# Kernel tuning notes

Hardware: AMD Instinct MI355X
Metric: run time of the kernel (lower is better)

Reference implementation:

```python
import jax, jax.numpy as jnp
import numpy as np

NUM_BLOCKS = 16  # 4x4 grid of 2x2 blocks over the 8x8 matrix
E_BLK, H_BLK = 4, 2
E_CROSS, H_CROSS = 64, 8
VOCAB = 32000
LN_EPS = 1e-5


def _mha(x, Wqkv, bqkv, Wo, bo, nheads):
    """torch nn.MultiheadAttention (batch_first, self-attn, eval mode).
    Returns (out [B,T,E], attn weights averaged over heads [B,T,T])."""
    B, T, E = x.shape
    Dh = E // nheads
    qkv = x @ Wqkv.T + bqkv                      # [B,T,3E]
    q, k, v = jnp.split(qkv, 3, axis=-1)
    sp = lambda t: t.reshape(B, T, nheads, Dh).transpose(0, 2, 1, 3)  # [B,H,T,Dh]
    q, k, v = sp(q), sp(k), sp(v)
    scale = 1.0 / float(np.sqrt(Dh))
    scores = jnp.einsum('bhqd,bhkd->bhqk', q, k) * scale
    attn = jax.nn.softmax(scores, axis=-1)
    out = jnp.einsum('bhqk,bhkd->bhqd', attn, v).transpose(0, 2, 1, 3).reshape(B, T, E)
    return out @ Wo.T + bo, attn.mean(axis=1)


def _layernorm(x, g, b):
    mu = x.mean(-1, keepdims=True)
    var = x.var(-1, keepdims=True)
    return (x - mu) * jax.lax.rsqrt(var + LN_EPS) * g + b


def _to_blocks(M):
    # [B,T,8,8] -> [B,T,16,4]; block i = (row_blk*4+col_blk), 2x2 flattened row-major
    B, T = M.shape[:2]
    return jnp.transpose(M.reshape(B, T, 4, 2, 4, 2), (0, 1, 2, 4, 3, 5)).reshape(B, T, 16, 4)


def _from_blocks(x):
    # [B,T,16,4] -> [B,T,8,8]
    B, T = x.shape[:2]
    return jnp.transpose(x.reshape(B, T, 4, 4, 2, 2), (0, 1, 2, 4, 3, 5)).reshape(B, T, 8, 8)


def setup_inputs() -> dict:
    key = jax.random.key(0)
    ks = jax.random.split(key, 24)
    B, T = 4, 1024
    s = 0.05
    return {
        'M': jax.random.normal(ks[0], (B, T, 8, 8), jnp.float32),
        'token_ids': jax.random.randint(ks[1], (B, T), 0, VOCAB, jnp.int64),
        # 16 per-block MHA param sets (stacked)
        'Wqkv_blk': jax.random.normal(ks[2], (NUM_BLOCKS, 3 * E_BLK, E_BLK), jnp.float32) * s,
        'bqkv_blk': jnp.zeros((NUM_BLOCKS, 3 * E_BLK), jnp.float32),
        'Wo_blk': jax.random.normal(ks[3], (NUM_BLOCKS, E_BLK, E_BLK), jnp.float32) * s,
        'bo_blk': jnp.zeros((NUM_BLOCKS, E_BLK), jnp.float32),
        # cross-block MHA
        'Wqkv_c': jax.random.normal(ks[4], (3 * E_CROSS, E_CROSS), jnp.float32) * s,
        'bqkv_c': jnp.zeros((3 * E_CROSS,), jnp.float32),
        'Wo_c': jax.random.normal(ks[5], (E_CROSS, E_CROSS), jnp.float32) * s,
        'bo_c': jnp.zeros((E_CROSS,), jnp.float32),
        # FFN 64 -> 256 -> 64
        'W1': jax.random.normal(ks[6], (256, 64), jnp.float32) * s,
        'b1': jnp.zeros((256,), jnp.float32),
        'W2': jax.random.normal(ks[7], (64, 256), jnp.float32) * s,
        'b2': jnp.zeros((64,), jnp.float32),
        # LayerNorms
        'g1': jnp.ones((64,), jnp.float32), 'be1': jnp.zeros((64,), jnp.float32),
        'g2': jnp.ones((64,), jnp.float32), 'be2': jnp.zeros((64,), jnp.float32),
        # DynamicBlockSensitivity params
        'sens_emb': jax.random.normal(ks[8], (VOCAB, NUM_BLOCKS), jnp.float32) * s,
        'sens_alpha': jax.random.normal(ks[9], (NUM_BLOCKS,), jnp.float32) * s,
    }


def reference(M, token_ids, Wqkv_blk, bqkv_blk, Wo_blk, bo_blk,
              Wqkv_c, bqkv_c, Wo_c, bo_c, W1, b1, W2, b2,
              g1, be1, g2, be2, sens_emb, sens_alpha):
    B, T = M.shape[:2]
    blocks = _to_blocks(M)                                # [B,T,16,4]
    x_blk = jnp.moveaxis(blocks, 2, 0)                    # [16,B,T,4]
    blk_out, _ = jax.vmap(lambda x, W, b, Wo, bo: _mha(x, W, b, Wo, bo, H_BLK))(
        x_blk, Wqkv_blk, bqkv_blk, Wo_blk, bo_blk)        # [16,B,T,4]
    all_blocks = jnp.moveaxis(blk_out, 0, 2).reshape(B, T, 64)
    cross_out, attn_w = _mha(all_blocks, Wqkv_c, bqkv_c, Wo_c, bo_c, H_CROSS)
    all_blocks = _layernorm(all_blocks + cross_out, g1, be1)
    ffn = jax.nn.gelu(all_blocks @ W1.T + b1, approximate=False) @ W2.T + b2
    all_blocks = _layernorm(all_blocks + ffn, g2, be2)
    # Dynamic block sensitivity: token embedding + attention-received modulation
    attn_recv = attn_w.mean(axis=1)                       # [B,T] attention each token receives
    sens = jax.nn.sigmoid(sens_emb[token_ids] + attn_recv[..., None] * sens_alpha)  # [B,T,16]
    new_blocks = blocks + (all_blocks.reshape(B, T, 16, 4) - blocks) * sens[..., None]
    return _from_blocks(new_blocks)
```

## Files before the change

kernel.cpp:

```cpp
#include <hip/hip_runtime.h>
#include <hip/hip_bf16.h>
#include <math.h>

#define BB 4
#define TT 1024
#define BT 4096

#define OFF_BLOCKS 0
#define OFF_QKVB   262144
#define OFF_RECVP  262144
#define OFF_ALLB   1048576
#define OFF_QKVC   1310720
#define OFF_LC     2097152
#define OFF_ACCC   2129920
#define OFF_LN1    2396160
#define OFF_PARAMS 2658304
#define WS_FLOATS  2708624

#define P_W1T    0
#define P_W2T    16384
#define P_WQCT   32768
#define P_WOCT   45056
#define P_WOBLK  49152
#define P_BOBLK  49408
#define P_BQC    49472
#define P_BOC    49664
#define P_G1     49728
#define P_BE1    49792
#define P_B1     49856
#define P_B2     50112
#define P_G2     50176
#define P_BE2    50240
#define P_SAL    50304
#define P_TOTAL  50320

__device__ inline float rcpf(float x) { return __builtin_amdgcn_rcpf(x); }

typedef _Float16 h2 __attribute__((ext_vector_type(2)));
typedef __fp16   fh2 __attribute__((ext_vector_type(2)));
typedef _Float16 h8v __attribute__((ext_vector_type(8)));
typedef float    f4v __attribute__((ext_vector_type(4)));

__device__ inline uint pkh(float a, float b) {
#if __has_builtin(__builtin_amdgcn_cvt_pkrtz)
  fh2 r = __builtin_amdgcn_cvt_pkrtz(a, b);
  return __builtin_bit_cast(uint, r);
#else
  h2 r = { (_Float16)a, (_Float16)b };
  return __builtin_bit_cast(uint, r);
#endif
}
__device__ inline h2 toh2(uint u) { return __builtin_bit_cast(h2, u); }

__device__ inline bool detect_bf16(const void* M) {
  const unsigned short* h = (const unsigned short*)M;
  unsigned short v = h[threadIdx.x & 63];
  int e = (v >> 7) & 0xff;
  unsigned long long m = __ballot((e >= 90) && (e <= 141));
  return __popcll(m) >= 58;
}

template <bool ISBF>
__device__ inline float ldf(const void* p, int i) {
  if (ISBF) return __bfloat162float(((const __hip_bfloat16*)p)[i]);
  else      return ((const float*)p)[i];
}

template <bool ISBF>
__device__ void prep2_body(
    const void* M, const void* Wqkv_blk, const void* bqkv_blk,
    const void* W1, const void* W2, const void* Wqkv_c, const void* Wo_c,
    const void* Wo_blk, const void* bo_blk, const void* bqkv_c, const void* bo_c,
    const void* g1, const void* be1, const void* b1, const void* b2,
    const void* g2, const void* be2, const void* sens_al,
    float* blocks, float* qkv_blk, float* params) {
  if (blockIdx.x < 256) {
    int g = blockIdx.x * 256 + threadIdx.x;
    int i = g >> 12, bt = g & 4095;
    int rb = i >> 2, cb = i & 3;
    float x[4];
    #pragma unroll
    for (int r = 0; r < 2; ++r)
      #pragma unroll
      for (int c = 0; c < 2; ++c)
        x[r*2+c] = ldf<ISBF>(M, bt*64 + (rb*2+r)*8 + cb*2 + c);
    float* bo = blocks + bt*64 + i*4;
    #pragma unroll
    for (int j = 0; j < 4; ++j) bo[j] = x[j];
    float* o = qkv_blk + (i*BT + bt) * 12;
    #pragma unroll
    for (int c = 0; c < 12; ++c) {
      float a = ldf<ISBF>(bqkv_blk, i*12 + c);
      #pragma unroll
      for (int j = 0; j < 4; ++j) a += ldf<ISBF>(Wqkv_blk, i*48 + c*4 + j) * x[j];
      o[c] = a;
    }
  } else {
    for (int o = (blockIdx.x - 256)*256 + threadIdx.x; o < P_TOTAL; o += 16*256) {
      float v;
      if      (o < 16384) { int j = o >> 8, h2_ = o & 255; v = ldf<ISBF>(W1, h2_*64 + j); }
      else if (o < 32768) { int q = o - 16384; int k = q >> 6, j = q & 63; v = ldf<ISBF>(W2, j*256 + k); }
      else if (o < 45056) { int q = o - 32768; int j = q / 192, c = q % 192; v = ldf<ISBF>(Wqkv_c, c*64 + j); }
      else if (o < 49152) { int q = o - 45056; int m = q >> 6, j = q & 63; v = ldf<ISBF>(Wo_c, j*64 + m); }
      else if (o < 49408) v = ldf<ISBF>(Wo_blk, o - 49152);
      else if (o < 49472) v = ldf<ISBF>(bo_blk, o - 49408);
      else if (o < 49664) v = ldf<ISBF>(bqkv_c, o - 49472);
      else if (o < 49728) v = ldf<ISBF>(bo_c,   o - 49664);
      else if (o < 49792) v = ldf<ISBF>(g1,     o - 49728);
      else if (o < 49856) v = ldf<ISBF>(be1,    o - 49792);
      else if (o < 50112) v = ldf<ISBF>(b1,     o - 49856);
      else if (o < 50176) v = ldf<ISBF>(b2,     o - 50112);
      else if (o < 50240) v = ldf<ISBF>(g2,     o - 50176);
      else if (o < 50304) v = ldf<ISBF>(be2,    o - 50240);
      else                v = ldf<ISBF>(sens_al, o - 50304);
      params[o] = v;
    }
  }
}

__global__ void __launch_bounds__(256) k_prep3(
    const void* __restrict__ M, const void* __restrict__ Wqkv_blk,
    const void* __restrict__ bqkv_blk,
    const void* __restrict__ W1, const void* __restrict__ W2,
    const void* __restrict__ Wqkv_c, const void* __restrict__ Wo_c,
    const void* __restrict__ Wo_blk, const void* __restrict__ bo_blk,
    const void* __restrict__ bqkv_c, const void* __restrict__ bo_c,
    const void* __restrict__ g1, const void* __restrict__ be1,
    const void* __restrict__ b1, const void* __restrict__ b2,
    const void* __restrict__ g2, const void* __restrict__ be2,
    const void* __restrict__ sens_al,
    float* __restrict__ blocks, float* __restrict__ qkv_blk,
    float* __restrict__ params) {
  if (detect_bf16(M))
    prep2_body<true >(M, Wqkv_blk, bqkv_blk, W1, W2, Wqkv_c, Wo_c, Wo_blk, bo_blk,
                      bqkv_c, bo_c, g1, be1, b1, b2, g2, be2, sens_al,
                      blocks, qkv_blk, params);
  else
    prep2_body<false>(M, Wqkv_blk, bqkv_blk, W1, W2, Wqkv_c, Wo_c, Wo_blk, bo_blk,
                      bqkv_c, bo_c, g1, be1, b1, b2, g2, be2, sens_al,
                      blocks, qkv_blk, params);
}

__global__ void __launch_bounds__(1024) k_blk5(
    const float* __restrict__ qkv_blk,
    const float* __restrict__ params,
    float* __restrict__ all_blocks) {
  __shared__ __align__(16) uint lds[16916];
  uint* kvu = lds;
  uint* vt  = lds + 4096;
  ushort* vt16 = (ushort*)vt;
  int bid = blockIdx.x;
  int qg = bid & 3, b = (bid >> 2) & 3, i = bid >> 4;
  int tid = threadIdx.x;
  int wv = tid >> 6, lane = tid & 63;
  int lq = lane & 15, g = lane >> 4;
  const float* slab = qkv_blk + (size_t)(i*BT + b*TT) * 12;
  {
    int r = tid;
    const float4* rp = (const float4*)(slab + (size_t)r*12);
    float4 x1 = rp[1], x2 = rp[2];
    uint v01 = pkh(x2.x, x2.y), v23 = pkh(x2.z, x2.w);
    *(uint4*)(kvu + r*4) = make_uint4(pkh(x1.x,x1.y), pkh(x1.z,x1.w), v01, v23);
    vt16[0*1032 + r] = (ushort)(v01 & 0xffffu);
    vt16[1*1032 + r] = (ushort)(v01 >> 16);
    vt16[2*1032 + r] = (ushort)(v23 & 0xffffu);
    vt16[3*1032 + r] = (ushort)(v23 >> 16);
    vt16[4*1032 + r] = (ushort)0x3C00;
  }
  int qrow = qg*256 + wv*16 + lq;
  float4 qv = *(const float4*)(slab + (size_t)qrow*12);
  const float S2L = 0.70710678f * 1.44269504f;
  uint pq01 = pkh(qv.x*S2L, qv.y*S2L);
  uint pq23 = pkh(qv.z*S2L, qv.w*S2L);
  uint4 bq0u = make_uint4(g == 0 ? pq01 : 0u, 0u, 0u, 0u);
  uint4 bq1u = make_uint4(0u, g == 0 ? pq23 : 0u, 0u, 0u);
  h8v B0 = __builtin_bit_cast(h8v, bq0u);
  h8v B1 = __builtin_bit_cast(h8v, bq1u);
  __syncthreads();
  uint* pt0 = lds + 6676 + (size_t)(wv*2 + 0)*320;
  uint* pt1 = lds + 6676 + (size_t)(wv*2 + 1)*320;
  f4v acc0 = {0.f, 0.f, 0.f, 0.f};
  f4v acc1 = {0.f, 0.f, 0.f, 0.f};
  for (int c = 0; c < 32; ++c) {
    int kb = c*32;
    #pragma unroll
    for (int t = 0; t < 2; ++t) {
      uint4 aku = *(const uint4*)(kvu + (size_t)(kb + t*16 + lq)*4);
      h8v AK = __builtin_bit_cast(h8v, aku);
      f4v z = {0.f, 0.f, 0.f, 0.f};
      f4v s0 = __builtin_amdgcn_mfma_f32_16x16x32_f16(AK, B0, z, 0, 0, 0);
      f4v s1 = __builtin_amdgcn_mfma_f32_16x16x32_f16(AK, B1, z, 0, 0, 0);
      uint a01 = pkh(exp2f(s0[0]), exp2f(s0[1]));
      uint a23 = pkh(exp2f(s0[2]), exp2f(s0[3]));
      uint c01 = pkh(exp2f(s1[0]), exp2f(s1[1]));
      uint c23 = pkh(exp2f(s1[2]), exp2f(s1[3]));
      *(uint2*)(pt0 + lq*20 + t*8 + g*2) = make_uint2(a01, a23);
      *(uint2*)(pt1 + lq*20 + t*8 + g*2) = make_uint2(c01, c23);
    }
    uint4 avu = make_uint4(0u, 0u, 0u, 0u);
    if (lq < 5) avu = *(const uint4*)(vt + (size_t)lq*516 + c*16 + g*4);
    h8v AV = __builtin_bit_cast(h8v, avu);
    h8v BP0 = __builtin_bit_cast(h8v, *(const uint4*)(pt0 + lq*20 + g*4));
    h8v BP1 = __builtin_bit_cast(h8v, *(const uint4*)(pt1 + lq*20 + g*4));
    acc0 = __builtin_amdgcn_mfma_f32_16x16x32_f16(AV, BP0, acc0, 0, 0, 0);
    acc1 = __builtin_amdgcn_mfma_f32_16x16x32_f16(AV, BP1, acc1, 0, 0, 0);
  }
  float l0 = __shfl(acc0[0], 16 + lq);
  float l1 = __shfl(acc1[0], 16 + lq);
  if (g == 0) {
    float inv0 = rcpf(l0), inv1 = rcpf(l1);
    float o[4] = { acc0[0]*inv0, acc0[1]*inv0, acc1[2]*inv1, acc1[3]*inv1 };
    const float* pWo = params + P_WOBLK + i*16;
    float4 outv;
    #pragma unroll
    for (int j = 0; j < 4; ++j) {
      float a = params[P_BOBLK + i*4 + j];
      #pragma unroll
      for (int m2 = 0; m2 < 4; ++m2) a += pWo[j*4 + m2] * o[m2];
      ((float*)&outv)[j] = a;
    }
    *(float4*)(all_blocks + (size_t)(b*TT + qrow)*64 + i*4) = outv;
  }
}

__global__ void __launch_bounds__(256) k_qkv_c3(
    const float* __restrict__ all_blocks,
    const float* __restrict__ params,
    float* __restrict__ qkv_c) {
  __shared__ __align__(16) uint wt[6912];
  int tid = threadIdx.x;
  int wv = tid >> 6, lane = tid & 63;
  int lq = lane & 15, g = lane >> 4;
  for (int o = tid; o < 6144; o += 256) {
    int c = o % 192, jp = o / 192;
    float w0 = params[P_WQCT + (2*jp    )*192 + c];
    float w1 = params[P_WQCT + (2*jp + 1)*192 + c];
    wt[c*36 + jp] = pkh(w0, w1);
  }
  int t0 = blockIdx.x * 16;
  const float* xr = all_blocks + (size_t)(t0 + lq)*64;
  uint4 a0u, a1u;
  {
    float4 x0 = *(const float4*)(xr + 8*g);
    float4 x1 = *(const float4*)(xr + 8*g + 4);
    a0u = make_uint4(pkh(x0.x,x0.y), pkh(x0.z,x0.w), pkh(x1.x,x1.y), pkh(x1.z,x1.w));
    float4 x2 = *(const float4*)(xr + 32 + 8*g);
    float4 x3 = *(const float4*)(xr + 32 + 8*g + 4);
    a1u = make_uint4(pkh(x2.x,x2.y), pkh(x2.z,x2.w), pkh(x3.x,x3.y), pkh(x3.z,x3.w));
  }
  h8v A0 = __builtin_bit_cast(h8v, a0u);
  h8v A1 = __builtin_bit_cast(h8v, a1u);
  __syncthreads();
  #pragma unroll
  for (int nt = 0; nt < 3; ++nt) {
    int ct = wv*3 + nt;
    int c = ct*16 + lq;
    h8v Bw0 = __builtin_bit_cast(h8v, *(const uint4*)(wt + c*36 + g*4));
    h8v Bw1 = __builtin_bit_cast(h8v, *(const uint4*)(wt + c*36 + 16 + g*4));
    f4v acc = {0.f, 0.f, 0.f, 0.f};
    acc = __builtin_amdgcn_mfma_f32_16x16x32_f16(A0, Bw0, acc, 0, 0, 0);
    acc = __builtin_amdgcn_mfma_f32_16x16x32_f16(A1, Bw1, acc, 0, 0, 0);
    float bias = params[P_BQC + c];
    #pragma unroll
    for (int r = 0; r < 4; ++r)
      qkv_c[(size_t)(t0 + 4*g + r)*192 + c] = acc[r] + bias;
  }
}

__global__ void __launch_bounds__(1024) k_cross12(
    const float* __restrict__ qkv_c,
    float* __restrict__ acc_c,
    float* __restrict__ recv_part) {
  __shared__ __align__(16) uint lds[24740];
  uint* Ku = lds;
  uint* Vt = lds + 4096;
  ushort* vt16 = (ushort*)Vt;
  uint* PT = lds + 8740;
  float* red = (float*)(lds + 18980);
  uint* qb_ = lds + 23716;
  float* qbf = (float*)qb_;
  int bid = blockIdx.x;
  int h = bid & 7, b = (bid >> 3) & 3, qg = bid >> 5;
  int tid = threadIdx.x;
  int wv = tid >> 6, lane = tid & 63;
  int lq = lane & 15, g = lane >> 4;
  int h8 = h*8;
  const float* base = qkv_c + (size_t)b*TT*192;
  {
    int r = tid;
    const float4* kp = (const float4*)(base + (size_t)r*192 + 64 + h8);
    const float4* vp = (const float4*)(base + (size_t)r*192 + 128 + h8);
    float4 k0 = kp[0], k1 = kp[1], v0 = vp[0], v1 = vp[1];
    *(uint4*)(Ku + r*4) = make_uint4(pkh(k0.x,k0.y), pkh(k0.z,k0.w),
                                     pkh(k1.x,k1.y), pkh(k1.z,k1.w));
    uint v01 = pkh(v0.x,v0.y), v23 = pkh(v0.z,v0.w);
    uint v45 = pkh(v1.x,v1.y), v67 = pkh(v1.z,v1.w);
    vt16[0*1032 + r] = (ushort)(v01 & 0xffffu);
    vt16[1*1032 + r] = (ushort)(v01 >> 16);
    vt16[2*1032 + r] = (ushort)(v23 & 0xffffu);
    vt16[3*1032 + r] = (ushort)(v23 >> 16);
    vt16[4*1032 + r] = (ushort)(v45 & 0xffffu);
    vt16[5*1032 + r] = (ushort)(v45 >> 16);
    vt16[6*1032 + r] = (ushort)(v67 & 0xffffu);
    vt16[7*1032 + r] = (ushort)(v67 >> 16);
    vt16[8*1032 + r] = (ushort)0x3C00;
  }
  int qpair = wv >> 2, ks = wv & 3;
  int qlA = qpair*32 + lq, qlB = qlA + 16;
  const float SCL = 0.35355339f * 1.44269504f;
  uint4 b0u = make_uint4(0u,0u,0u,0u), b1u = make_uint4(0u,0u,0u,0u);
  if (g == 0) {
    int qA = qg*128 + qlA, qB = qA + 16;
    const float4* pa = (const float4*)(base + (size_t)qA*192 + h8);
    const float4* pb = (const float4*)(base + (size_t)qB*192 + h8);
    float4 a0 = pa[0], a1 = pa[1], c0 = pb[0], c1 = pb[1];
    b0u = make_uint4(pkh(a0.x*SCL,a0.y*SCL), pkh(a0.z*SCL,a0.w*SCL),
                     pkh(a1.x*SCL,a1.y*SCL), pkh(a1.z*SCL,a1.w*SCL));
    b1u = make_uint4(pkh(c0.x*SCL,c0.y*SCL), pkh(c0.z*SCL,c0.w*SCL),
                     pkh(c1.x*SCL,c1.y*SCL), pkh(c1.z*SCL,c1.w*SCL));
    if (ks == 0) {
      *(uint4*)(qb_ + qlA*8) = b0u;
      *(uint4*)(qb_ + qlB*8) = b1u;
    }
  }
  h8v B0 = __builtin_bit_cast(h8v, b0u);
  h8v B1 = __builtin_bit_cast(h8v, b1u);
  __syncthreads();
  uint* pt0 = PT + (size_t)(wv*2)*320;
  uint* pt1 = pt0 + 320;
  f4v acc0 = {0.f,0.f,0.f,0.f};
  f4v acc1 = {0.f,0.f,0.f,0.f};
  const uint4 zu4 = make_uint4(0u,0u,0u,0u);
  for (int c = ks*8; c < ks*8 + 8; ++c) {
    #pragma unroll
    for (int t = 0; t < 2; ++t) {
      uint4 aku = (g == 0) ? *(const uint4*)(Ku + (size_t)(c*32 + t*16 + lq)*4) : zu4;
      h8v AK = __builtin_bit_cast(h8v, aku);
      f4v z = {0.f,0.f,0.f,0.f};
      f4v s0 = __builtin_amdgcn_mfma_f32_16x16x32_f16(AK, B0, z, 0, 0, 0);
      f4v s1 = __builtin_amdgcn_mfma_f32_16x16x32_f16(AK, B1, z, 0, 0, 0);
      *(uint2*)(pt0 + lq*20 + t*8 + g*2) =
          make_uint2(pkh(exp2f(s0[0]), exp2f(s0[1])), pkh(exp2f(s0[2]), exp2f(s0[3])));
      *(uint2*)(pt1 + lq*20 + t*8 + g*2) =
          make_uint2(pkh(exp2f(s1[0]), exp2f(s1[1])), pkh(exp2f(s1[2]), exp2f(s1[3])));
    }
    uint4 avu = (lq < 9) ? *(const uint4*)(Vt + (size_t)lq*516 + c*16 + g*4) : zu4;
    h8v AV = __builtin_bit_cast(h8v, avu);
    h8v BP0 = __builtin_bit_cast(h8v, *(const uint4*)(pt0 + lq*20 + g*4));
    h8v BP1 = __builtin_bit_cast(h8v, *(const uint4*)(pt1 + lq*20 + g*4));
    acc0 = __builtin_amdgcn_mfma_f32_16x16x32_f16(AV, BP0, acc0, 0, 0, 0);
    acc1 = __builtin_amdgcn_mfma_f32_16x16x32_f16(AV, BP1, acc1, 0, 0, 0);
  }
  {
    float* rA = red + (size_t)qlA*37 + ks*9;
    float* rB = red + (size_t)qlB*37 + ks*9;
    if (g == 0) {
      rA[0]=acc0[0]; rA[1]=acc0[1]; rA[2]=acc0[2]; rA[3]=acc0[3];
      rB[0]=acc1[0]; rB[1]=acc1[1]; rB[2]=acc1[2]; rB[3]=acc1[3];
    } else if (g == 1) {
      rA[4]=acc0[0]; rA[5]=acc0[1]; rA[6]=acc0[2]; rA[7]=acc0[3];
      rB[4]=acc1[0]; rB[5]=acc1[1]; rB[6]=acc1[2]; rB[7]=acc1[3];
    } else if (g == 2) {
      rA[8]=acc0[0];
      rB[8]=acc1[0];
    }
  }
  __syncthreads();
  if (tid < 128) {
    int q = tid;
    const float* rr = red + (size_t)q*37;
    float ls = rr[8] + rr[17] + rr[26] + rr[35];
    float od[8];
    #pragma unroll
    for (int d = 0; d < 8; ++d)
      od[d] = rr[d] + rr[9+d] + rr[18+d] + rr[27+d];
    float invl = rcpf(ls);
    int idx = (b*8 + h)*TT + qg*128 + q;
    float4 o0 = { od[0]*invl, od[1]*invl, od[2]*invl, od[3]*invl };
    float4 o1 = { od[4]*invl, od[5]*invl, od[6]*invl, od[7]*invl };
    float4* op = (float4*)(acc_c + (size_t)idx*8);
    op[0] = o0; op[1] = o1;
    qbf[q*8 + 4] = -__log2f(ls);
  }
  __syncthreads();
  {
    int src = h*8 + qg;
    #pragma unroll
    for (int it = 0; it < 4; ++it) {
      int kt = wv*4 + it;
      uint4 aku = (g == 0) ? *(const uint4*)(Ku + (size_t)(kt*16 + lq)*4) : zu4;
      h8v AK = __builtin_bit_cast(h8v, aku);
      f4v racc = {0.f,0.f,0.f,0.f};
      for (int qt = 0; qt < 8; ++qt) {
        uint4 bqu = (g == 0) ? *(const uint4*)(qb_ + (size_t)(qt*16 + lq)*8) : zu4;
        h8v BQ = __builtin_bit_cast(h8v, bqu);
        f4v z = {0.f,0.f,0.f,0.f};
        f4v s = __builtin_amdgcn_mfma_f32_16x16x32_f16(AK, BQ, z, 0, 0, 0);
        float mq = qbf[(size_t)(qt*16 + lq)*8 + 4];
        racc[0] += exp2f(s[0] + mq);
        racc[1] += exp2f(s[1] + mq);
        racc[2] += exp2f(s[2] + mq);
        racc[3] += exp2f(s[3] + mq);
      }
      #pragma unroll
      for (int off = 1; off < 16; off <<= 1) {
        racc[0] += __shfl_xor(racc[0], off);
        racc[1] += __shfl_xor(racc[1], off);
        racc[2] += __shfl_xor(racc[2], off);
        racc[3] += __shfl_xor(racc[3], off);
      }
      if (lq == 0) {
        int k = kt*16 + g*4;
        size_t bk = ((size_t)(b*1024 + k))*64 + src;
        recv_part[bk      ] = racc[0];
        recv_part[bk +  64] = racc[1];
        recv_part[bk + 128] = racc[2];
        recv_part[bk + 192] = racc[3];
      }
    }
  }
}

__global__ void __launch_bounds__(256) k_fin(
    const float* __restrict__ all_blocks,
    const float* __restrict__ acc_c,
    const float* __restrict__ params,
    float* __restrict__ ln1) {
  __shared__ float pvs[4*64];
  int tt = threadIdx.x >> 6, j = threadIdx.x & 63;
  int t = blockIdx.x*4 + tt;
  int b = t >> 10, tl = t & 1023;
  int h = j >> 3;
  int idx = (b*8 + h)*TT + tl;
  pvs[tt*64 + j] = acc_c[idx*8 + (j & 7)];
  __syncthreads();
  float a = params[P_BOC + j];
  const float* WoT = params + P_WOCT;
  const float* p = pvs + tt*64;
  #pragma unroll 8
  for (int m = 0; m < 64; ++m) a += WoT[m*64 + j] * p[m];
  float x = all_blocks[t*64 + j] + a;
  float s = x, s2 = x*x;
  #pragma unroll
  for (int off = 32; off; off >>= 1) { s += __shfl_xor(s, off); s2 += __shfl_xor(s2, off); }
  float mu  = s  * (1.f/64.f);
  float var = s2 * (1.f/64.f) - mu*mu;
  float y = (x - mu) * rsqrtf(var + 1e-5f) * params[P_G1 + j] + params[P_BE1 + j];
  ln1[t*64 + j] = y;
}

template <bool ISBF>
__device__ void ffn_body(
    const float* ln1, const float* params, const float* blocks,
    const int* tok32, const float* recv_part, const void* sens_emb, void* out,
    float* w, float* ld2, float* hbuf) {
  int tid = threadIdx.x;
  int t0 = blockIdx.x * 8;
  int wv = tid >> 6, lane = tid & 63;
  float recv;
  {
    int t = t0 + wv, b = t >> 10, k = t & 1023;
    const float* rp = recv_part + ((size_t)(b*1024 + k))*64;
    float s = rp[lane];
    #pragma unroll
    for (int off = 32; off; off >>= 1) s += __shfl_xor(s, off);
    recv = s * (1.f/8192.f);
  }
  ld2[lane*8 + wv] = ln1[(t0 + wv)*64 + lane];
  {
    const float4* src = (const float4*)(params + P_W1T);
    float4* dst = (float4*)w;
    #pragma unroll
    for (int i = tid; i < 4096; i += 512) dst[i] = src[i];
  }
  __syncthreads();
  {
    int g = tid >> 8, u = tid & 255;
    float a0, a1, a2, a3;
    a0 = a1 = a2 = a3 = params[P_B1 + u];
    #pragma unroll 8
    for (int j = 0; j < 64; ++j) {
      float wj = w[j*256 + u];
      float4 xj = *(const float4*)(ld2 + j*8 + g*4);
      a0 += wj*xj.x; a1 += wj*xj.y; a2 += wj*xj.z; a3 += wj*xj.w;
    }
    float av[4] = {a0, a1, a2, a3};
    float4 hv;
    #pragma unroll
    for (int t2 = 0; t2 < 4; ++t2) {
      float v = av[t2];
      float u2 = 1.5957691f*v + 0.07135481f*v*v*v;
      ((float*)&hv)[t2] = v * rcpf(1.f + __expf(-u2));
    }
    *(float4*)(hbuf + u*8 + g*4) = hv;
  }
  __syncthreads();
  {
    const float4* src = (const float4*)(params + P_W2T);
    float4* dst = (float4*)w;
    #pragma unroll
    for (int i = tid; i < 4096; i += 512) dst[i] = src[i];
  }
  __syncthreads();
  float yp[8] = {0.f,0.f,0.f,0.f,0.f,0.f,0.f,0.f};
  {
    int j = lane, k0 = wv*32;
    #pragma unroll 8
    for (int k = k0; k < k0 + 32; ++k) {
      float wkj = w[k*64 + j];
      float4 h03 = *(const float4*)(hbuf + k*8);
      float4 h47 = *(const float4*)(hbuf + k*8 + 4);
      yp[0] += wkj*h03.x; yp[1] += wkj*h03.y; yp[2] += wkj*h03.z; yp[3] += wkj*h03.w;
      yp[4] += wkj*h47.x; yp[5] += wkj*h47.y; yp[6] += wkj*h47.z; yp[7] += wkj*h47.w;
    }
  }
  __syncthreads();
  float* red2 = w;
  {
    #pragma unroll
    for (int t2 = 0; t2 < 8; ++t2) red2[wv*520 + t2*64 + lane] = yp[t2];
  }
  __syncthreads();
  int j = lane;
  int tok = wv;
  int t = t0 + tok, b = t >> 10;
  float y = params[P_B2 + j];
  #pragma unroll
  for (int wq = 0; wq < 8; ++wq) y += red2[wq*520 + tok*64 + j];
  float z = ld2[j*8 + tok] + y;
  float s = z, s2 = z*z;
  #pragma unroll
  for (int off = 32; off; off >>= 1) { s += __shfl_xor(s, off); s2 += __shfl_xor(s2, off); }
  float mu  = s  * (1.f/64.f);
  float var = s2 * (1.f/64.f) - mu*mu;
  float y2 = (z - mu) * rsqrtf(var + 1e-5f) * params[P_G2 + j] + params[P_BE2 + j];
  bool is64 = ((tok32[1] | tok32[3] | tok32[5] | tok32[7]) == 0);
  int tk = is64 ? tok32[t*2] : tok32[t];
  int i = j >> 2, e = j & 3;
  float sv = ldf<ISBF>(sens_emb, tk*16 + i) + recv * params[P_SAL + i];
  float sg = rcpf(1.f + __expf(-sv));
  float blk = blocks[t*64 + j];
  float nb = blk + (y2 - blk) * sg;
  int rb = i >> 2, cb = i & 3, r = e >> 1, c = e & 1;
  int oidx = t*64 + (rb*2 + r)*8 + cb*2 + c;
  if (ISBF) ((__hip_bfloat16*)out)[oidx] = __float2bfloat16(nb);
  else      ((float*)out)[oidx] = nb;
}

__global__ void __launch_bounds__(512) k_ffn_out3(
    const void* __restrict__ M,
    const float* __restrict__ ln1,
    const float* __restrict__ params,
    const float* __restrict__ blocks,
    const int* __restrict__ tok32,
    const float* __restrict__ recv_part,
    const void* __restrict__ sens_emb,
    void* __restrict__ out) {
  __shared__ float w[16384];
  __shared__ float ld2[512];
  __shared__ float hbuf[2048];
  if (detect_bf16(M))
    ffn_body<true >(ln1, params, blocks, tok32, recv_part, sens_emb, out, w, ld2, hbuf);
  else
    ffn_body<false>(ln1, params, blocks, tok32, recv_part, sens_emb, out, w, ld2, hbuf);
}

extern "C" void kernel_launch(void* const* d_in, const int* in_sizes, int n_in,
                              void* d_out, int out_size, void* d_ws, size_t ws_size,
                              hipStream_t stream) {
  const void* M        = d_in[0];
  const int*  tok      = (const int*)d_in[1];
  const void* Wqkv_blk = d_in[2];
  const void* bqkv_blk = d_in[3];
  const void* Wo_blk   = d_in[4];
  const void* bo_blk   = d_in[5];
  const void* Wqkv_c   = d_in[6];
  const void* bqkv_c   = d_in[7];
  const void* Wo_c     = d_in[8];
  const void* bo_c     = d_in[9];
  const void* W1       = d_in[10];
  const void* b1       = d_in[11];
  const void* W2       = d_in[12];
  const void* b2       = d_in[13];
  const void* g1       = d_in[14];
  const void* be1      = d_in[15];
  const void* g2i      = d_in[16];
  const void* be2      = d_in[17];
  const void* sens_emb = d_in[18];
  const void* sens_al  = d_in[19];

  float* ws = (float*)d_ws;
  float* blocks    = ws + OFF_BLOCKS;
  float* qkv_blk   = ws + OFF_QKVB;
  float* recv_part = ws + OFF_RECVP;
  float* all_blk   = ws + OFF_ALLB;
  float* qkv_c     = ws + OFF_QKVC;
  float* acc_c     = ws + OFF_ACCC;
  float* ln1       = ws + OFF_LN1;
  float* params    = ws + OFF_PARAMS;

  k_prep3<<<272, 256, 0, stream>>>(M, Wqkv_blk, bqkv_blk, W1, W2, Wqkv_c, Wo_c,
                                   Wo_blk, bo_blk, bqkv_c, bo_c, g1, be1, b1, b2,
                                   g2i, be2, sens_al, blocks, qkv_blk, params);
  k_blk5<<<256, 1024, 0, stream>>>(qkv_blk, params, all_blk);
  k_qkv_c3<<<256, 256, 0, stream>>>(all_blk, params, qkv_c);
  k_cross12<<<256, 1024, 0, stream>>>(qkv_c, acc_c, recv_part);
  k_fin<<<1024, 256, 0, stream>>>(all_blk, acc_c, params, ln1);
  k_ffn_out3<<<512, 512, 0, stream>>>(M, ln1, params, blocks, tok, recv_part,
                                      sens_emb, (void*)d_out);
}
```

Measured before the change: 192.6 us.

## Fuse cross-attn output projection and LayerNorm into FFN kernel; use raw exp2 intrinsics

Merges the k_fin kernel (Wo projection of the cross-attention output, residual add, first LayerNorm) into the FFN/output kernel. Each wave now computes the LN1 row for its token and writes it straight into shared memory, so one launch and the round trip of the ln1 buffer through global memory go away. It also swaps exp2f and __log2f for the raw AMDGCN exp2 and log intrinsics in the attention kernels, which skips the range-handling wrappers. The risk is lower precision for extreme inputs, plus more shared memory and longer serial work per FFN block.

```diff
diff --git a/kernel.cpp b/kernel.cpp
--- a/kernel.cpp
+++ b/kernel.cpp
@@ -35,6 +35,21 @@
 #define P_TOTAL  50320
 
 __device__ inline float rcpf(float x) { return __builtin_amdgcn_rcpf(x); }
+
+__device__ inline float ex2(float x) {
+#if __has_builtin(__builtin_amdgcn_exp2f)
+  return __builtin_amdgcn_exp2f(x);
+#else
+  return exp2f(x);
+#endif
+}
+__device__ inline float lg2(float x) {
+#if __has_builtin(__builtin_amdgcn_logf)
+  return __builtin_amdgcn_logf(x);
+#else
+  return __log2f(x);
+#endif
+}
 
 typedef _Float16 h2 __attribute__((ext_vector_type(2)));
 typedef __fp16   fh2 __attribute__((ext_vector_type(2)));
@@ -190,10 +205,10 @@
       f4v z = {0.f, 0.f, 0.f, 0.f};
       f4v s0 = __builtin_amdgcn_mfma_f32_16x16x32_f16(AK, B0, z, 0, 0, 0);
       f4v s1 = __builtin_amdgcn_mfma_f32_16x16x32_f16(AK, B1, z, 0, 0, 0);
-      uint a01 = pkh(exp2f(s0[0]), exp2f(s0[1]));
-      uint a23 = pkh(exp2f(s0[2]), exp2f(s0[3]));
-      uint c01 = pkh(exp2f(s1[0]), exp2f(s1[1]));
-      uint c23 = pkh(exp2f(s1[2]), exp2f(s1[3]));
+      uint a01 = pkh(ex2(s0[0]), ex2(s0[1]));
+      uint a23 = pkh(ex2(s0[2]), ex2(s0[3]));
+      uint c01 = pkh(ex2(s1[0]), ex2(s1[1]));
+      uint c23 = pkh(ex2(s1[2]), ex2(s1[3]));
       *(uint2*)(pt0 + lq*20 + t*8 + g*2) = make_uint2(a01, a23);
       *(uint2*)(pt1 + lq*20 + t*8 + g*2) = make_uint2(c01, c23);
     }
@@ -340,9 +355,9 @@
       f4v s0 = __builtin_amdgcn_mfma_f32_16x16x32_f16(AK, B0, z, 0, 0, 0);
       f4v s1 = __builtin_amdgcn_mfma_f32_16x16x32_f16(AK, B1, z, 0, 0, 0);
       *(uint2*)(pt0 + lq*20 + t*8 + g*2) =
-          make_uint2(pkh(exp2f(s0[0]), exp2f(s0[1])), pkh(exp2f(s0[2]), exp2f(s0[3])));
+          make_uint2(pkh(ex2(s0[0]), ex2(s0[1])), pkh(ex2(s0[2]), ex2(s0[3])));
       *(uint2*)(pt1 + lq*20 + t*8 + g*2) =
-          make_uint2(pkh(exp2f(s1[0]), exp2f(s1[1])), pkh(exp2f(s1[2]), exp2f(s1[3])));
+          make_uint2(pkh(ex2(s1[0]), ex2(s1[1])), pkh(ex2(s1[2]), ex2(s1[3])));
     }
     uint4 avu = (lq < 9) ? *(const uint4*)(Vt + (size_t)lq*516 + c*16 + g*4) : zu4;
     h8v AV = __builtin_bit_cast(h8v, avu);
@@ -380,7 +395,7 @@
     float4 o1 = { od[4]*invl, od[5]*invl, od[6]*invl, od[7]*invl };
     float4* op = (float4*)(acc_c + (size_t)idx*8);
     op[0] = o0; op[1] = o1;
-    qbf[q*8 + 4] = -__log2f(ls);
+    qbf[q*8 + 4] = -lg2(ls);
   }
   __syncthreads();
   {
@@ -397,10 +412,10 @@
         f4v z = {0.f,0.f,0.f,0.f};
         f4v s = __builtin_amdgcn_mfma_f32_16x16x32_f16(AK, BQ, z, 0, 0, 0);
         float mq = qbf[(size_t)(qt*16 + lq)*8 + 4];
-        racc[0] += exp2f(s[0] + mq);
-        racc[1] += exp2f(s[1] + mq);
-        racc[2] += exp2f(s[2] + mq);
-        racc[3] += exp2f(s[3] + mq);
+        racc[0] += ex2(s[0] + mq);
+        racc[1] += ex2(s[1] + mq);
+        racc[2] += ex2(s[2] + mq);
+        racc[3] += ex2(s[3] + mq);
       }
       #pragma unroll
       for (int off = 1; off < 16; off <<= 1) {
@@ -421,52 +436,43 @@
   }
 }
 
-__global__ void __launch_bounds__(256) k_fin(
-    const float* __restrict__ all_blocks,
-    const float* __restrict__ acc_c,
-    const float* __restrict__ params,
-    float* __restrict__ ln1) {
-  __shared__ float pvs[4*64];
-  int tt = threadIdx.x >> 6, j = threadIdx.x & 63;
-  int t = blockIdx.x*4 + tt;
-  int b = t >> 10, tl = t & 1023;
-  int h = j >> 3;
-  int idx = (b*8 + h)*TT + tl;
-  pvs[tt*64 + j] = acc_c[idx*8 + (j & 7)];
-  __syncthreads();
-  float a = params[P_BOC + j];
-  const float* WoT = params + P_WOCT;
-  const float* p = pvs + tt*64;
-  #pragma unroll 8
-  for (int m = 0; m < 64; ++m) a += WoT[m*64 + j] * p[m];
-  float x = all_blocks[t*64 + j] + a;
-  float s = x, s2 = x*x;
-  #pragma unroll
-  for (int off = 32; off; off >>= 1) { s += __shfl_xor(s, off); s2 += __shfl_xor(s2, off); }
-  float mu  = s  * (1.f/64.f);
-  float var = s2 * (1.f/64.f) - mu*mu;
-  float y = (x - mu) * rsqrtf(var + 1e-5f) * params[P_G1 + j] + params[P_BE1 + j];
-  ln1[t*64 + j] = y;
-}
-
 template <bool ISBF>
-__device__ void ffn_body(
-    const float* ln1, const float* params, const float* blocks,
+__device__ void finffn_body(
+    const float* all_blocks, const float* acc_c,
+    const float* params, const float* blocks,
     const int* tok32, const float* recv_part, const void* sens_emb, void* out,
-    float* w, float* ld2, float* hbuf) {
+    float* w, float* ld2, float* hbuf, float* pvs) {
   int tid = threadIdx.x;
   int t0 = blockIdx.x * 8;
   int wv = tid >> 6, lane = tid & 63;
+  int t = t0 + wv, b = t >> 10, tl = t & 1023;
+  {
+    int h = lane >> 3;
+    int idx = (b*8 + h)*TT + tl;
+    pvs[wv*64 + lane] = acc_c[(size_t)idx*8 + (lane & 7)];
+    float a = params[P_BOC + lane];
+    const float* WoT = params + P_WOCT;
+    const float* p = pvs + wv*64;
+    #pragma unroll 8
+    for (int m = 0; m < 64; ++m) a += WoT[m*64 + lane] * p[m];
+    float x = all_blocks[(size_t)t*64 + lane] + a;
+    float s = x, s2 = x*x;
+    #pragma unroll
+    for (int off = 32; off; off >>= 1) { s += __shfl_xor(s, off); s2 += __shfl_xor(s2, off); }
+    float mu  = s  * (1.f/64.f);
+    float var = s2 * (1.f/64.f) - mu*mu;
+    float y = (x - mu) * rsqrtf(var + 1e-5f) * params[P_G1 + lane] + params[P_BE1 + lane];
+    ld2[lane*8 + wv] = y;
+  }
   float recv;
   {
-    int t = t0 + wv, b = t >> 10, k = t & 1023;
+    int k = t & 1023;
     const float* rp = recv_part + ((size_t)(b*1024 + k))*64;
     float s = rp[lane];
     #pragma unroll
     for (int off = 32; off; off >>= 1) s += __shfl_xor(s, off);
     recv = s * (1.f/8192.f);
   }
-  ld2[lane*8 + wv] = ln1[(t0 + wv)*64 + lane];
   {
     const float4* src = (const float4*)(params + P_W1T);
     float4* dst = (float4*)w;
@@ -523,7 +529,6 @@
   __syncthreads();
   int j = lane;
   int tok = wv;
-  int t = t0 + tok, b = t >> 10;
   float y = params[P_B2 + j];
   #pragma unroll
   for (int wq = 0; wq < 8; ++wq) y += red2[wq*520 + tok*64 + j];
@@ -547,9 +552,10 @@
   else      ((float*)out)[oidx] = nb;
 }
 
-__global__ void __launch_bounds__(512) k_ffn_out3(
+__global__ void __launch_bounds__(512) k_finffn(
     const void* __restrict__ M,
-    const float* __restrict__ ln1,
+    const float* __restrict__ all_blocks,
+    const float* __restrict__ acc_c,
     const float* __restrict__ params,
     const float* __restrict__ blocks,
     const int* __restrict__ tok32,
@@ -559,10 +565,13 @@
   __shared__ float w[16384];
   __shared__ float ld2[512];
   __shared__ float hbuf[2048];
+  __shared__ float pvs[512];
   if (detect_bf16(M))
-    ffn_body<true >(ln1, params, blocks, tok32, recv_part, sens_emb, out, w, ld2, hbuf);
+    finffn_body<true >(all_blocks, acc_c, params, blocks, tok32, recv_part,
+                       sens_emb, out, w, ld2, hbuf, pvs);
   else
-    ffn_body<false>(ln1, params, blocks, tok32, recv_part, sens_emb, out, w, ld2, hbuf);
+    finffn_body<false>(all_blocks, acc_c, params, blocks, tok32, recv_part,
+                       sens_emb, out, w, ld2, hbuf, pvs);
 }
 
 extern "C" void kernel_launch(void* const* d_in, const int* in_sizes, int n_in,
@@ -596,7 +605,6 @@
   float* all_blk   = ws + OFF_ALLB;
   float* qkv_c     = ws + OFF_QKVC;
   float* acc_c     = ws + OFF_ACCC;
-  float* ln1       = ws + OFF_LN1;
   float* params    = ws + OFF_PARAMS;
 
   k_prep3<<<272, 256, 0, stream>>>(M, Wqkv_blk, bqkv_blk, W1, W2, Wqkv_c, Wo_c,
@@ -605,7 +613,6 @@
   k_blk5<<<256, 1024, 0, stream>>>(qkv_blk, params, all_blk);
   k_qkv_c3<<<256, 256, 0, stream>>>(all_blk, params, qkv_c);
   k_cross12<<<256, 1024, 0, stream>>>(qkv_c, acc_c, recv_part);
-  k_fin<<<1024, 256, 0, stream>>>(all_blk, acc_c, params, ln1);
-  k_ffn_out3<<<512, 512, 0, stream>>>(M, ln1, params, blocks, tok, recv_part,
-                                      sens_emb, (void*)d_out);
-}
+  k_finffn<<<512, 512, 0, stream>>>(M, all_blk, acc_c, params, blocks, tok,
+                                    recv_part, sens_emb, (void*)d_out);
+}
```

Result: faster. 173.8 us (-9.7%).
